# Kernel tuning notes

Hardware: AMD Instinct MI355X
Metric: run time of the kernel (lower is better)

## Reference

```python
import jax, jax.numpy as jnp
import numpy as np

B, N, E = 16, 2048, 1_048_576          # graphs, residues per graph, total edges
IN_C, DIM, OUT_C, ENC_H, N_ATOMS = 256, 128, 6, 100, 20
NT = B * N


def setup_inputs() -> dict:
    key = jax.random.key(0)
    ks = jax.random.split(key, 24)
    s = 0.02
    x_res = jax.random.normal(ks[0], (NT, IN_C), jnp.float32)
    coords = jax.random.normal(ks[1], (NT, 3), jnp.float32)
    batch = jnp.repeat(jnp.arange(B, dtype=jnp.int32), N)
    src = jax.random.randint(ks[2], (E,), 0, NT, dtype=jnp.int32)
    dst = (src // N) * N + jax.random.randint(ks[3], (E,), 0, N, dtype=jnp.int32)
    edge_index = jnp.stack([src, dst])  # intra-graph edges, global node ids
    return {
        'x_res': x_res, 'coords': coords,
        'edge_index': edge_index, 'batch': batch,
        'bn_gamma': jnp.ones((IN_C,), jnp.float32),
        'bn_beta': jnp.zeros((IN_C,), jnp.float32),
        'W1': s * jax.random.normal(ks[4], (IN_C, 2 * DIM), jnp.float32),
        'b1': jnp.zeros((2 * DIM,), jnp.float32),
        'W2': s * jax.random.normal(ks[5], (2 * DIM, DIM), jnp.float32),
        'b2': jnp.zeros((DIM,), jnp.float32),
        'W3': s * jax.random.normal(ks[6], (DIM, N_ATOMS), jnp.float32),
        'b3': jnp.zeros((N_ATOMS,), jnp.float32),
        'embed': s * jax.random.normal(ks[7], (N_ATOMS + 1, DIM), jnp.float32),
        'W_msg': s * jax.random.normal(ks[8], (DIM, DIM), jnp.float32),
        'b_msg': jnp.zeros((DIM,), jnp.float32),
        'w_coor': s * jax.random.normal(ks[9], (DIM, 3), jnp.float32),
        'A1': s * jax.random.normal(ks[10], (DIM, ENC_H), jnp.float32),
        'a1': jnp.zeros((ENC_H,), jnp.float32),
        'A2': s * jax.random.normal(ks[11], (ENC_H, OUT_C), jnp.float32),
        'a2': jnp.zeros((OUT_C,), jnp.float32),
        'dyt_alpha': jnp.float32(0.5),
        'dyt_w': jnp.ones((OUT_C,), jnp.float32),
        'dyt_b': jnp.zeros((OUT_C,), jnp.float32),
    }


def reference(x_res, coords, edge_index, batch,
              bn_gamma, bn_beta, W1, b1, W2, b2, W3, b3,
              embed, W_msg, b_msg, w_coor,
              A1, a1, A2, a2, dyt_alpha, dyt_w, dyt_b):
    gelu = lambda v: jax.nn.gelu(v, approximate=False)
    # BatchNorm1d (train-mode batch stats, biased var, eps=1e-5); dropout is identity in eval
    mu = x_res.mean(0)
    var = x_res.var(0)
    xn = (x_res - mu) / jnp.sqrt(var + 1e-5) * bn_gamma + bn_beta
    # input2atomids MLP -> argmax atom ids
    h1 = gelu(xn @ W1 + b1)
    h2 = gelu(h1 @ W2 + b2)
    logits = h2 @ W3 + b3
    ids = jnp.argmax(logits, axis=-1)          # [NT]
    ids_b = ids.reshape(B, N)                  # equal-sized graphs -> no padding needed
    coords_b = coords.reshape(B, N, 3)
    # vectorized edge-list -> dense per-graph adjacency scatter
    g = batch[edge_index[0]]                   # graph id per edge
    ls = edge_index[0] - g * N                 # local src index
    ld = edge_index[1] - g * N                 # local dst index
    same = batch[edge_index[1]] == g           # keep intra-graph edges only
    adj = jnp.zeros((B, N, N), jnp.bool_).at[g, ls, ld].max(same)
    # GotenNet stand-in: embed atom ids, one adjacency-masked aggregation layer
    emb_ids = jnp.where(ids_b < 0, N_ATOMS, ids_b)   # -1 pad -> pad embedding row
    h = embed[emb_ids]                          # [B,N,DIM]
    adjf = adj.astype(h.dtype)
    deg = jnp.maximum(adjf.sum(-1, keepdims=True), 1.0)
    m = jnp.einsum('bij,bjd->bid', adjf, h) / deg
    hout = gelu((h + m) @ W_msg + b_msg)        # invariant features [B,N,DIM]
    coors_out = coords_b + jnp.tanh(hout @ w_coor)
    # un-pad / flatten back to node list, then out_angles head
    z = hout.reshape(NT, DIM)
    t = gelu(z @ A1 + a1)
    t = gelu(t @ A2 + a2)
    t = jnp.tanh(dyt_alpha * t) * dyt_w + dyt_b  # DynamicTanh (channels_last)
    angles = jnp.tanh(t)                         # [NT, OUT_C]
    return angles, z, coors_out
```

## Files before the change

### kernel.cpp

```cpp
#include <hip/hip_runtime.h>
#include <hip/hip_bf16.h>
#include <math.h>

#define Bg 16
#define Nn 2048
#define Ee (1<<20)
#define NT (Bg*Nn)
#define INC 256
#define DIMd 128
#define OUTC 6
#define ENCH 100
#define NATOMS 20

typedef __attribute__((ext_vector_type(8))) short bf16x8;
typedef __attribute__((ext_vector_type(4))) float f32x4;

__device__ __forceinline__ float gelu_f(float x){
    return 0.5f*x*(1.0f+erff(x*0.70710678118654752440f));
}
__device__ __forceinline__ unsigned short f2b(float f){
    __hip_bfloat16 h = __float2bfloat16(f);
    return *(unsigned short*)&h;
}
__device__ __forceinline__ float b2f(unsigned short u){
    unsigned v = ((unsigned)u)<<16;
    return __uint_as_float(v);
}
__device__ __forceinline__ void splitf(float v, unsigned short& hi, unsigned short& lo){
    unsigned short h = f2b(v);
    hi = h; lo = f2b(v - b2f(h));
}

__global__ __launch_bounds__(256) void prep0_k(const float* __restrict__ x,
    float* __restrict__ stats, const float* __restrict__ W1,
    const float* __restrict__ W2, const float* __restrict__ Wm,
    const float* __restrict__ A1, short* __restrict__ w1th, short* __restrict__ w1tl,
    short* __restrict__ w2th, short* __restrict__ w2tl,
    short* __restrict__ wmth, short* __restrict__ wmtl,
    short* __restrict__ a1th, short* __restrict__ a1tl)
{
    int bx = blockIdx.x, tid = threadIdx.x;
    if(bx < 256){
        int c = tid;
        int r0 = bx * 128;
        const float* p = x + (size_t)r0*INC + c;
        float s = 0.f, s2 = 0.f;
        #pragma unroll 8
        for(int r=0;r<128;r++){ float v = p[(size_t)r*INC]; s += v; s2 += v*v; }
        atomicAdd(&stats[c], s);
        atomicAdd(&stats[INC+c], s2);
    } else {
        int gid = (bx-256)*256 + tid;
        unsigned short hi, lo;
        for(int l=gid;l<65536;l+=16384){ int n=l>>8,k=l&255;
            splitf(W1[(size_t)k*256+n],hi,lo); w1th[l]=(short)hi; w1tl[l]=(short)lo; }
        for(int l=gid;l<32768;l+=16384){ int n=l>>8,k=l&255;
            splitf(W2[(size_t)k*128+n],hi,lo); w2th[l]=(short)hi; w2tl[l]=(short)lo; }
        for(int l=gid;l<16384;l+=16384){ int n=l>>7,k=l&127;
            splitf(Wm[(size_t)k*128+n],hi,lo); wmth[l]=(short)hi; wmtl[l]=(short)lo; }
        for(int l=gid;l<16384;l+=16384){ int n=l>>7,k=l&127;
            float v=(n<ENCH)? A1[(size_t)k*ENCH+n] : 0.f;
            splitf(v,hi,lo); a1th[l]=(short)hi; a1tl[l]=(short)lo; }
    }
}

__global__ __launch_bounds__(256) void gemm1_adj_k(const float* __restrict__ x,
    const float* __restrict__ stats, const float* __restrict__ gamma,
    const float* __restrict__ beta, const short* __restrict__ w1th,
    const short* __restrict__ w1tl, const float* __restrict__ b1,
    unsigned short* __restrict__ h1h, unsigned short* __restrict__ h1l,
    const int* __restrict__ ei, unsigned* __restrict__ mask)
{
    __shared__ float sc[256], sh[256];
    __shared__ short sAh[64*40], sAl[64*40];
    __shared__ short sBh[256*40], sBl[256*40];
    int tid = threadIdx.x;
    {
        float mu  = stats[tid]*(1.0f/NT);
        float var = stats[256+tid]*(1.0f/NT) - mu*mu;
        float s = gamma[tid]/sqrtf(var + 1e-5f);
        sc[tid] = s; sh[tid] = beta[tid] - mu*s;
    }
    int row0 = blockIdx.x*64;
    int lane = tid&63, w = tid>>6;
    int ln = lane&15, quad = lane>>4;
    int m0w = (w&1)*32, n0b = (w>>1)*128;
    f32x4 acc[2][8];
    #pragma unroll
    for(int i=0;i<2;i++)
        #pragma unroll
        for(int j=0;j<8;j++) acc[i][j] = (f32x4){0.f,0.f,0.f,0.f};
    __syncthreads();
    for(int k0=0;k0<256;k0+=32){
        #pragma unroll
        for(int i=0;i<2;i++){
            int id = tid + i*256; int r = id>>3, kq = (id&7)*4;
            float4 vx = *(const float4*)&x[(size_t)(row0+r)*256 + k0+kq];
            int k = k0+kq;
            float v0 = vx.x*sc[k]+sh[k],   v1 = vx.y*sc[k+1]+sh[k+1];
            float v2 = vx.z*sc[k+2]+sh[k+2], v3 = vx.w*sc[k+3]+sh[k+3];
            ushort4 hi, lo;
            splitf(v0,hi.x,lo.x); splitf(v1,hi.y,lo.y);
            splitf(v2,hi.z,lo.z); splitf(v3,hi.w,lo.w);
            *(ushort4*)&sAh[r*40+kq] = hi;
            *(ushort4*)&sAl[r*40+kq] = lo;
        }
        #pragma unroll
        for(int i=0;i<8;i++){
            int id = tid + i*256; int plane = id>>10, cid = id&1023;
            int r = cid>>2, c = cid&3;
            const short* src = (plane? w1tl : w1th) + (size_t)r*256 + k0 + c*8;
            short* dst = (plane? sBl : sBh) + r*40 + c*8;
            *(bf16x8*)dst = *(const bf16x8*)src;
        }
        __syncthreads();
        bf16x8 ah[2], al[2];
        #pragma unroll
        for(int tm=0;tm<2;tm++){
            ah[tm] = *(const bf16x8*)&sAh[(m0w+tm*16+ln)*40 + quad*8];
            al[tm] = *(const bf16x8*)&sAl[(m0w+tm*16+ln)*40 + quad*8];
        }
        #pragma unroll
        for(int tn=0;tn<8;tn++){
            bf16x8 bh = *(const bf16x8*)&sBh[(n0b+tn*16+ln)*40 + quad*8];
            bf16x8 bl = *(const bf16x8*)&sBl[(n0b+tn*16+ln)*40 + quad*8];
            #pragma unroll
            for(int tm=0;tm<2;tm++){
                acc[tm][tn] = __builtin_amdgcn_mfma_f32_16x16x32_bf16(al[tm], bh, acc[tm][tn], 0,0,0);
                acc[tm][tn] = __builtin_amdgcn_mfma_f32_16x16x32_bf16(ah[tm], bl, acc[tm][tn], 0,0,0);
                acc[tm][tn] = __builtin_amdgcn_mfma_f32_16x16x32_bf16(ah[tm], bh, acc[tm][tn], 0,0,0);
            }
        }
        __syncthreads();
    }
    #pragma unroll
    for(int tn=0;tn<8;tn++){
        int col = n0b + tn*16 + ln;
        float bias = b1[col];
        #pragma unroll
        for(int tm=0;tm<2;tm++){
            int rowb = row0 + m0w + tm*16 + quad*4;
            #pragma unroll
            for(int r=0;r<4;r++){
                float hv = gelu_f(acc[tm][tn][r] + bias);
                unsigned short hi, lo;
                splitf(hv, hi, lo);
                h1h[(size_t)(rowb+r)*256 + col] = hi;
                h1l[(size_t)(rowb+r)*256 + col] = lo;
            }
        }
    }
    int ebase = blockIdx.x*2048;
    #pragma unroll
    for(int i=0;i<8;i++){
        int e = ebase + i*256 + tid;
        int s = ei[e], d = ei[Ee+e];
        if((s>>11) == (d>>11)){
            int ld = d & (Nn-1);
            atomicOr(&mask[(size_t)s*64 + (ld>>5)], 1u<<(ld&31));
        }
    }
}

__global__ __launch_bounds__(256) void gemm23_mfma(
    const unsigned short* __restrict__ h1h, const unsigned short* __restrict__ h1l,
    const short* __restrict__ w2th, const short* __restrict__ w2tl,
    const float* __restrict__ b2, const float* __restrict__ W3,
    const float* __restrict__ b3, int* __restrict__ ids)
{
    __shared__ short sAh[64*40], sAl[64*40];
    __shared__ short sBh[128*40], sBl[128*40];
    __shared__ float h2s[64*132];
    __shared__ float lgs[64*20];
    int tid = threadIdx.x;
    int row0 = blockIdx.x*64;
    int lane = tid&63, w = tid>>6;
    int ln = lane&15, quad = lane>>4;
    int m0w = (w&1)*32, n0w = (w>>1)*64;
    f32x4 acc[2][4];
    #pragma unroll
    for(int i=0;i<2;i++)
        #pragma unroll
        for(int j=0;j<4;j++) acc[i][j] = (f32x4){0.f,0.f,0.f,0.f};
    for(int k0=0;k0<256;k0+=32){
        #pragma unroll
        for(int i=0;i<2;i++){
            int id = tid + i*256; int plane = id>>8, cid = id&255;
            int r = cid>>2, c = cid&3;
            const unsigned short* src = (plane? h1l : h1h)
                                        + (size_t)(row0+r)*256 + k0 + c*8;
            short* dst = (plane? sAl : sAh) + r*40 + c*8;
            *(bf16x8*)dst = *(const bf16x8*)src;
        }
        #pragma unroll
        for(int i=0;i<4;i++){
            int id = tid + i*256; int plane = id>>9, cid = id&511;
            int r = cid>>2, c = cid&3;
            const short* src = (plane? w2tl : w2th) + (size_t)r*256 + k0 + c*8;
            short* dst = (plane? sBl : sBh) + r*40 + c*8;
            *(bf16x8*)dst = *(const bf16x8*)src;
        }
        __syncthreads();
        bf16x8 ah[2], al[2];
        #pragma unroll
        for(int tm=0;tm<2;tm++){
            ah[tm] = *(const bf16x8*)&sAh[(m0w+tm*16+ln)*40 + quad*8];
            al[tm] = *(const bf16x8*)&sAl[(m0w+tm*16+ln)*40 + quad*8];
        }
        #pragma unroll
        for(int tn=0;tn<4;tn++){
            bf16x8 bh = *(const bf16x8*)&sBh[(n0w+tn*16+ln)*40 + quad*8];
            bf16x8 bl = *(const bf16x8*)&sBl[(n0w+tn*16+ln)*40 + quad*8];
            #pragma unroll
            for(int tm=0;tm<2;tm++){
                acc[tm][tn] = __builtin_amdgcn_mfma_f32_16x16x32_bf16(al[tm], bh, acc[tm][tn], 0,0,0);
                acc[tm][tn] = __builtin_amdgcn_mfma_f32_16x16x32_bf16(ah[tm], bl, acc[tm][tn], 0,0,0);
                acc[tm][tn] = __builtin_amdgcn_mfma_f32_16x16x32_bf16(ah[tm], bh, acc[tm][tn], 0,0,0);
            }
        }
        __syncthreads();
    }
    #pragma unroll
    for(int tn=0;tn<4;tn++){
        int col = n0w + tn*16 + ln;
        float bias = b2[col];
        #pragma unroll
        for(int tm=0;tm<2;tm++){
            int rb = m0w + tm*16 + quad*4;
            #pragma unroll
            for(int r=0;r<4;r++)
                h2s[(rb+r)*132 + col] = gelu_f(acc[tm][tn][r] + bias);
        }
    }
    float* w3s = (float*)sBh;
    for(int l=tid;l<2560;l+=256) w3s[l] = W3[l];
    __syncthreads();
    int n = tid>>2, q = tid&3;
    float lg[5] = {};
    #pragma unroll 4
    for(int k=0;k<128;k++){
        float h = h2s[n*132+k];
        #pragma unroll
        for(int a=0;a<5;a++) lg[a] += h*w3s[k*20 + q*5 + a];
    }
    #pragma unroll
    for(int a=0;a<5;a++) lgs[n*20 + q*5 + a] = lg[a] + b3[q*5+a];
    __syncthreads();
    if(tid<64){
        float best = lgs[tid*20]; int bi = 0;
        #pragma unroll
        for(int a=1;a<20;a++){ float v2 = lgs[tid*20+a]; if(v2>best){best=v2;bi=a;} }
        ids[row0+tid] = bi;
    }
}

__global__ __launch_bounds__(256) void msg3_k(
    const int* __restrict__ ids, const unsigned* __restrict__ mask,
    const float* __restrict__ embed,
    const short* __restrict__ wmth, const short* __restrict__ wmtl,
    const float* __restrict__ b_msg, const float* __restrict__ w_coor,
    const short* __restrict__ a1th, const short* __restrict__ a1tl,
    const float* __restrict__ a1v, const float* __restrict__ A2,
    const float* __restrict__ a2v, const float* __restrict__ dalpha,
    const float* __restrict__ dw, const float* __restrict__ db,
    const float* __restrict__ coords, float* __restrict__ out_ang,
    float* __restrict__ out_z, float* __restrict__ out_co)
{
    __shared__ unsigned short v_bf[64*136];
    __shared__ unsigned short houts[64*136];
    __shared__ __align__(16) unsigned char arena[20480];
    __shared__ float s_bm[128], s_wc[384], s_A2[624], s_a1[104];
    __shared__ float s_dyt[16], s_a2[8];

    unsigned*       ind = (unsigned*)arena;
    unsigned char*  sid = arena + 5120;
    float*          emb = (float*)(arena + 7168);
    short*          sBh = (short*)arena;
    short*          sBl = (short*)(arena + 10240);

    int tid = threadIdx.x;
    int row0 = blockIdx.x*64;
    int g = blockIdx.x>>5, tile = blockIdx.x&31;
    int lane = tid&63, w = tid>>6;
    int ln = lane&15, quad = lane>>4;
    int m0w = (w&1)*32, n0w = (w>>1)*64;

    for(int l=tid;l<NATOMS*128;l+=256) emb[l] = embed[l];
    #pragma unroll
    for(int i=0;i<8;i++){ int j = tid + i*256; sid[j] = (unsigned char)ids[g*Nn + j]; }
    if(tid<128) s_bm[tid] = b_msg[tid];
    if(tid<104) s_a1[tid] = (tid<ENCH) ? a1v[tid] : 0.f;
    for(int l=tid;l<384;l+=256) s_wc[l] = w_coor[l];
    for(int l=tid;l<624;l+=256) s_A2[l] = (l<600) ? A2[l] : 0.f;
    if(tid==0)  s_dyt[0] = dalpha[0];
    if(tid<6){ s_dyt[1+tid] = dw[tid]; s_dyt[8+tid] = db[tid]; }
    if(tid<8)  s_a2[tid] = (tid<6) ? a2v[tid] : 0.f;

    int node = tid>>2, p = tid&3;
    const unsigned* mrow = &mask[((size_t)(row0 + node))*64 + p*16];
    uint4 mm0 = *(const uint4*)&mrow[0];
    uint4 mm1 = *(const uint4*)&mrow[4];
    uint4 mm2 = *(const uint4*)&mrow[8];
    uint4 mm3 = *(const uint4*)&mrow[12];
    __syncthreads();

    for(int wp=w; wp<32; wp+=4){
        int a = sid[wp*64 + lane];
        #pragma unroll
        for(int atom=0; atom<NATOMS; atom++){
            unsigned long long bm = __ballot(a==atom);
            if(lane<2) ind[atom*64 + wp*2 + lane] = (unsigned)(bm >> (32*lane));
        }
    }
    __syncthreads();

    unsigned mw[16];
    *(uint4*)&mw[0]=mm0; *(uint4*)&mw[4]=mm1; *(uint4*)&mw[8]=mm2; *(uint4*)&mw[12]=mm3;
    int degi = 0;
    #pragma unroll
    for(int w2=0;w2<16;w2++) degi += __popc(mw[w2]);
    float cnt[NATOMS];
    #pragma unroll
    for(int a=0;a<NATOMS;a++){
        int c = 0;
        const unsigned* ia = &ind[a*64 + p*16];
        #pragma unroll
        for(int w2=0;w2<16;w2++) c += __popc(mw[w2] & ia[w2]);
        cnt[a] = (float)c;
    }
    #pragma unroll
    for(int a=0;a<NATOMS;a++){
        cnt[a] += __shfl_xor(cnt[a],1,64);
        cnt[a] += __shfl_xor(cnt[a],2,64);
    }
    float deg = (float)degi;
    deg += __shfl_xor(deg,1,64);
    deg += __shfl_xor(deg,2,64);

    {
        float inv = 1.0f / fmaxf(deg, 1.0f);
        int oid = sid[tile*64 + node];
        int d0 = p*32;
        float vv[32];
        #pragma unroll
        for(int d=0;d<32;d++) vv[d]=0.f;
        #pragma unroll
        for(int a=0;a<NATOMS;a++){
            float ca = cnt[a];
            const float* ea = &emb[a*128 + d0];
            #pragma unroll
            for(int d=0;d<32;d+=4){
                float4 e = *(const float4*)&ea[d];
                vv[d]+=ca*e.x; vv[d+1]+=ca*e.y; vv[d+2]+=ca*e.z; vv[d+3]+=ca*e.w;
            }
        }
        const float* eo = &emb[oid*128 + d0];
        unsigned short* dst = &v_bf[node*136 + d0];
        #pragma unroll
        for(int d=0;d<32;d+=4){
            float4 e = *(const float4*)&eo[d];
            ushort4 o;
            o.x = f2b(e.x + vv[d]*inv);
            o.y = f2b(e.y + vv[d+1]*inv);
            o.z = f2b(e.z + vv[d+2]*inv);
            o.w = f2b(e.w + vv[d+3]*inv);
            *(ushort4*)&dst[d] = o;
        }
    }
    __syncthreads();

    f32x4 acc[2][4];
    #pragma unroll
    for(int i=0;i<2;i++)
        #pragma unroll
        for(int j=0;j<4;j++) acc[i][j] = (f32x4){0.f,0.f,0.f,0.f};
    for(int k0=0;k0<128;k0+=32){
        #pragma unroll
        for(int i=0;i<4;i++){
            int id = tid + i*256; int plane = id>>9, cid = id&511;
            int r = cid>>2, c = cid&3;
            const short* src = (plane? wmtl : wmth) + (size_t)r*128 + k0 + c*8;
            short* dst = (plane? sBl : sBh) + r*40 + c*8;
            *(bf16x8*)dst = *(const bf16x8*)src;
        }
        __syncthreads();
        bf16x8 av[2];
        #pragma unroll
        for(int tm=0;tm<2;tm++)
            av[tm] = *(const bf16x8*)&v_bf[(m0w+tm*16+ln)*136 + k0 + quad*8];
        #pragma unroll
        for(int tn=0;tn<4;tn++){
            bf16x8 bh = *(const bf16x8*)&sBh[(n0w+tn*16+ln)*40 + quad*8];
            bf16x8 bl = *(const bf16x8*)&sBl[(n0w+tn*16+ln)*40 + quad*8];
            #pragma unroll
            for(int tm=0;tm<2;tm++){
                acc[tm][tn] = __builtin_amdgcn_mfma_f32_16x16x32_bf16(av[tm], bl, acc[tm][tn], 0,0,0);
                acc[tm][tn] = __builtin_amdgcn_mfma_f32_16x16x32_bf16(av[tm], bh, acc[tm][tn], 0,0,0);
            }
        }
        __syncthreads();
    }
    #pragma unroll
    for(int tn=0;tn<4;tn++){
        int col = n0w + tn*16 + ln;
        float bias = s_bm[col];
        #pragma unroll
        for(int tm=0;tm<2;tm++){
            int mb2 = m0w + tm*16 + quad*4;
            #pragma unroll
            for(int r=0;r<4;r++){
                float hv = gelu_f(acc[tm][tn][r] + bias);
                out_z[(size_t)(row0+mb2+r)*128 + col] = hv;
                houts[(mb2+r)*136 + col] = f2b(hv);
            }
        }
    }
    __syncthreads();

    {
        float d0=0.f, d1=0.f, d2=0.f;
        int kb = p*32;
        #pragma unroll
        for(int k=0;k<32;k+=4){
            ushort4 hv = *(const ushort4*)&houts[node*136 + kb + k];
            float h0=b2f(hv.x),h1=b2f(hv.y),h2=b2f(hv.z),h3=b2f(hv.w);
            const float* wc = &s_wc[(kb+k)*3];
            d0 += h0*wc[0]+h1*wc[3]+h2*wc[6]+h3*wc[9];
            d1 += h0*wc[1]+h1*wc[4]+h2*wc[7]+h3*wc[10];
            d2 += h0*wc[2]+h1*wc[5]+h2*wc[8]+h3*wc[11];
        }
        d0 += __shfl_xor(d0,1,64); d0 += __shfl_xor(d0,2,64);
        d1 += __shfl_xor(d1,1,64); d1 += __shfl_xor(d1,2,64);
        d2 += __shfl_xor(d2,1,64); d2 += __shfl_xor(d2,2,64);
        if(p==0){
            size_t o = (size_t)(row0+node)*3;
            out_co[o+0] = coords[o+0] + tanhf(d0);
            out_co[o+1] = coords[o+1] + tanhf(d1);
            out_co[o+2] = coords[o+2] + tanhf(d2);
        }
    }

    f32x4 acc2[2][4];
    #pragma unroll
    for(int i=0;i<2;i++)
        #pragma unroll
        for(int j=0;j<4;j++) acc2[i][j] = (f32x4){0.f,0.f,0.f,0.f};
    for(int k0=0;k0<128;k0+=32){
        __syncthreads();
        #pragma unroll
        for(int i=0;i<4;i++){
            int id = tid + i*256; int plane = id>>9, cid = id&511;
            int r = cid>>2, c = cid&3;
            const short* src = (plane? a1tl : a1th) + (size_t)r*128 + k0 + c*8;
            short* dst = (plane? sBl : sBh) + r*40 + c*8;
            *(bf16x8*)dst = *(const bf16x8*)src;
        }
        __syncthreads();
        bf16x8 ah[2];
        #pragma unroll
        for(int tm=0;tm<2;tm++)
            ah[tm] = *(const bf16x8*)&houts[(m0w+tm*16+ln)*136 + k0 + quad*8];
        #pragma unroll
        for(int tn=0;tn<4;tn++){
            bf16x8 bh = *(const bf16x8*)&sBh[(n0w+tn*16+ln)*40 + quad*8];
            bf16x8 bl = *(const bf16x8*)&sBl[(n0w+tn*16+ln)*40 + quad*8];
            #pragma unroll
            for(int tm=0;tm<2;tm++){
                acc2[tm][tn] = __builtin_amdgcn_mfma_f32_16x16x32_bf16(ah[tm], bl, acc2[tm][tn], 0,0,0);
                acc2[tm][tn] = __builtin_amdgcn_mfma_f32_16x16x32_bf16(ah[tm], bh, acc2[tm][tn], 0,0,0);
            }
        }
    }
    __syncthreads();
    unsigned short* t1s = houts;
    #pragma unroll
    for(int tn=0;tn<4;tn++){
        int col = n0w + tn*16 + ln;
        if(col < 104){
            float bias = s_a1[col];
            #pragma unroll
            for(int tm=0;tm<2;tm++){
                int mb2 = m0w + tm*16 + quad*4;
                #pragma unroll
                for(int r=0;r<4;r++)
                    t1s[(mb2+r)*104 + col] = f2b(gelu_f(acc2[tm][tn][r] + bias));
            }
        }
    }
    __syncthreads();

    {
        int g0 = (p<2) ? p*7 : 14+(p-2)*6;
        int gcount = (p<2) ? 7 : 6;
        float s[6] = {0.f,0.f,0.f,0.f,0.f,0.f};
        for(int gg=0; gg<gcount; gg++){
            int kb = (g0+gg)*4;
            ushort4 tv = *(const ushort4*)&t1s[node*104 + kb];
            float u0=b2f(tv.x), u1=b2f(tv.y), u2=b2f(tv.z), u3=b2f(tv.w);
            #pragma unroll
            for(int j=0;j<6;j++)
                s[j] += u0*s_A2[kb*6+j] + u1*s_A2[(kb+1)*6+j]
                      + u2*s_A2[(kb+2)*6+j] + u3*s_A2[(kb+3)*6+j];
        }
        #pragma unroll
        for(int j=0;j<6;j++){ s[j]+=__shfl_xor(s[j],1,64); s[j]+=__shfl_xor(s[j],2,64); }
        if(p<2){
            size_t o = (size_t)(row0+node)*6 + p*3;
            #pragma unroll
            for(int jj=0;jj<3;jj++){
                int j = p*3+jj;
                float t2v = gelu_f(s[j] + s_a2[j]);
                float uu = tanhf(s_dyt[0]*t2v)*s_dyt[1+j] + s_dyt[8+j];
                out_ang[o+jj] = tanhf(uu);
            }
        }
    }
}

extern "C" void kernel_launch(void* const* d_in, const int* in_sizes, int n_in,
                              void* d_out, int out_size, void* d_ws, size_t ws_size,
                              hipStream_t stream) {
    const float* x      = (const float*)d_in[0];
    const float* coords = (const float*)d_in[1];
    const int*   ei     = (const int*)d_in[2];
    const float* gamma  = (const float*)d_in[4];
    const float* beta   = (const float*)d_in[5];
    const float* W1     = (const float*)d_in[6];
    const float* b1     = (const float*)d_in[7];
    const float* W2     = (const float*)d_in[8];
    const float* b2     = (const float*)d_in[9];
    const float* W3     = (const float*)d_in[10];
    const float* b3     = (const float*)d_in[11];
    const float* embed  = (const float*)d_in[12];
    const float* W_msg  = (const float*)d_in[13];
    const float* b_msg  = (const float*)d_in[14];
    const float* w_coor = (const float*)d_in[15];
    const float* A1     = (const float*)d_in[16];
    const float* a1v    = (const float*)d_in[17];
    const float* A2     = (const float*)d_in[18];
    const float* a2v    = (const float*)d_in[19];
    const float* dalpha = (const float*)d_in[20];
    const float* dw     = (const float*)d_in[21];
    const float* db     = (const float*)d_in[22];

    char* ws = (char*)d_ws;
    int*      ids   = (int*)ws;
    float*    stats = (float*)(ws + 131072);
    short*    w1th  = (short*)(ws + 262144);
    short*    w1tl  = w1th + 65536;
    short*    w2th  = w1tl + 65536;
    short*    w2tl  = w2th + 32768;
    short*    wmth  = w2tl + 32768;
    short*    wmtl  = wmth + 16384;
    short*    a1th  = wmtl + 16384;
    short*    a1tl  = a1th + 16384;
    unsigned* mask  = (unsigned*)(ws + (1<<20));
    unsigned short* h1h = (unsigned short*)(ws + (size_t)10*1048576);
    unsigned short* h1l = (unsigned short*)(ws + (size_t)27*1048576);

    float* out_ang = (float*)d_out;
    float* out_z   = out_ang + (size_t)NT*OUTC;
    float* out_co  = out_z   + (size_t)NT*DIMd;

    hipMemsetAsync(stats, 0, 2*INC*sizeof(float), stream);
    hipMemsetAsync(mask, 0, (size_t)NT*64*sizeof(unsigned), stream);
    prep0_k<<<320, 256, 0, stream>>>(x, stats, W1, W2, W_msg, A1,
        w1th, w1tl, w2th, w2tl, wmth, wmtl, a1th, a1tl);
    gemm1_adj_k<<<512, 256, 0, stream>>>(x, stats, gamma, beta, w1th, w1tl, b1,
        h1h, h1l, ei, mask);
    gemm23_mfma<<<512, 256, 0, stream>>>(h1h, h1l, w2th, w2tl, b2, W3, b3, ids);
    msg3_k<<<512, 256, 0, stream>>>(ids, mask, embed, wmth, wmtl, b_msg, w_coor,
        a1th, a1tl, a1v, A2, a2v, dalpha, dw, db, coords, out_ang, out_z, out_co);
}
```

Before: 271.9 us.

## Bin edges per 64-node tile and build adjacency masks in LDS; register-prefetch GEMM tiles

Measured after the change: 253.9 us. -6.6%, faster.

```diff
diff --git a/kernel.cpp b/kernel.cpp
--- a/kernel.cpp
+++ b/kernel.cpp
@@ -11,6 +11,7 @@
 #define OUTC 6
 #define ENCH 100
 #define NATOMS 20
+#define BINCAP 3072
 
 typedef __attribute__((ext_vector_type(8))) short bf16x8;
 typedef __attribute__((ext_vector_type(4))) float f32x4;
@@ -64,12 +65,13 @@
     }
 }
 
-__global__ __launch_bounds__(256) void gemm1_adj_k(const float* __restrict__ x,
+__global__ __launch_bounds__(256) void gemm1_scat_k(const float* __restrict__ x,
     const float* __restrict__ stats, const float* __restrict__ gamma,
     const float* __restrict__ beta, const short* __restrict__ w1th,
     const short* __restrict__ w1tl, const float* __restrict__ b1,
     unsigned short* __restrict__ h1h, unsigned short* __restrict__ h1l,
-    const int* __restrict__ ei, unsigned* __restrict__ mask)
+    const int* __restrict__ ei, unsigned* __restrict__ ecnt,
+    unsigned* __restrict__ earena)
 {
     __shared__ float sc[256], sh[256];
     __shared__ short sAh[64*40], sAl[64*40];
@@ -90,15 +92,23 @@
     for(int i=0;i<2;i++)
         #pragma unroll
         for(int j=0;j<8;j++) acc[i][j] = (f32x4){0.f,0.f,0.f,0.f};
+
+    float4 xa[2]; bf16x8 wb[8];
+    #pragma unroll
+    for(int i=0;i<2;i++){ int id=tid+i*256; int r=id>>3,kq=(id&7)*4;
+        xa[i] = *(const float4*)&x[(size_t)(row0+r)*256 + kq]; }
+    #pragma unroll
+    for(int i=0;i<8;i++){ int id=tid+i*256; int plane=id>>10,cid=id&1023;
+        int r=cid>>2,c=cid&3;
+        wb[i] = *(const bf16x8*)((plane? w1tl:w1th) + (size_t)r*256 + c*8); }
     __syncthreads();
     for(int k0=0;k0<256;k0+=32){
         #pragma unroll
         for(int i=0;i<2;i++){
             int id = tid + i*256; int r = id>>3, kq = (id&7)*4;
-            float4 vx = *(const float4*)&x[(size_t)(row0+r)*256 + k0+kq];
             int k = k0+kq;
-            float v0 = vx.x*sc[k]+sh[k],   v1 = vx.y*sc[k+1]+sh[k+1];
-            float v2 = vx.z*sc[k+2]+sh[k+2], v3 = vx.w*sc[k+3]+sh[k+3];
+            float v0 = xa[i].x*sc[k]+sh[k],   v1 = xa[i].y*sc[k+1]+sh[k+1];
+            float v2 = xa[i].z*sc[k+2]+sh[k+2], v3 = xa[i].w*sc[k+3]+sh[k+3];
             ushort4 hi, lo;
             splitf(v0,hi.x,lo.x); splitf(v1,hi.y,lo.y);
             splitf(v2,hi.z,lo.z); splitf(v3,hi.w,lo.w);
@@ -109,11 +119,18 @@
         for(int i=0;i<8;i++){
             int id = tid + i*256; int plane = id>>10, cid = id&1023;
             int r = cid>>2, c = cid&3;
-            const short* src = (plane? w1tl : w1th) + (size_t)r*256 + k0 + c*8;
-            short* dst = (plane? sBl : sBh) + r*40 + c*8;
-            *(bf16x8*)dst = *(const bf16x8*)src;
-        }
-        __syncthreads();
+            *(bf16x8*)((plane? sBl : sBh) + r*40 + c*8) = wb[i];
+        }
+        __syncthreads();
+        if(k0 < 224){
+            #pragma unroll
+            for(int i=0;i<2;i++){ int id=tid+i*256; int r=id>>3,kq=(id&7)*4;
+                xa[i] = *(const float4*)&x[(size_t)(row0+r)*256 + k0+32+kq]; }
+            #pragma unroll
+            for(int i=0;i<8;i++){ int id=tid+i*256; int plane=id>>10,cid=id&1023;
+                int r=cid>>2,c=cid&3;
+                wb[i] = *(const bf16x8*)((plane? w1tl:w1th) + (size_t)r*256 + k0+32 + c*8); }
+        }
         bf16x8 ah[2], al[2];
         #pragma unroll
         for(int tm=0;tm<2;tm++){
@@ -150,14 +167,38 @@
             }
         }
     }
-    int ebase = blockIdx.x*2048;
-    #pragma unroll
-    for(int i=0;i<8;i++){
-        int e = ebase + i*256 + tid;
-        int s = ei[e], d = ei[Ee+e];
-        if((s>>11) == (d>>11)){
-            int ld = d & (Nn-1);
-            atomicOr(&mask[(size_t)s*64 + (ld>>5)], 1u<<(ld&31));
+    if(blockIdx.x < 128){
+        __syncthreads();
+        unsigned* lcnt  = (unsigned*)sAh;
+        unsigned* gbase = ((unsigned*)sAh) + 512;
+        for(int l=tid; l<512; l+=256) lcnt[l] = 0;
+        __syncthreads();
+        int ebase = blockIdx.x * 8192;
+        #pragma unroll 8
+        for(int i=0;i<32;i++){
+            int e = ebase + i*256 + tid;
+            int s = ei[e], d = ei[Ee+e];
+            if((s>>11)==(d>>11)) atomicAdd(&lcnt[s>>6], 1u);
+        }
+        __syncthreads();
+        for(int l=tid; l<512; l+=256){
+            unsigned c = lcnt[l];
+            gbase[l] = c ? atomicAdd(&ecnt[l], c) : 0u;
+            lcnt[l] = 0;
+        }
+        __syncthreads();
+        #pragma unroll 8
+        for(int i=0;i<32;i++){
+            int e = ebase + i*256 + tid;
+            int s = ei[e], d = ei[Ee+e];
+            if((s>>11)==(d>>11)){
+                int bin = s>>6;
+                unsigned r = atomicAdd(&lcnt[bin], 1u);
+                unsigned pos = gbase[bin] + r;
+                if(pos < BINCAP)
+                    earena[(size_t)bin*BINCAP + pos] =
+                        ((unsigned)(s&63)<<11) | (unsigned)(d&2047);
+            }
         }
     }
 }
@@ -182,25 +223,42 @@
     for(int i=0;i<2;i++)
         #pragma unroll
         for(int j=0;j<4;j++) acc[i][j] = (f32x4){0.f,0.f,0.f,0.f};
+
+    bf16x8 ha[2], wb[4];
+    #pragma unroll
+    for(int i=0;i<2;i++){ int id=tid+i*256; int plane=id>>8,cid=id&255;
+        int r=cid>>2,c=cid&3;
+        ha[i] = *(const bf16x8*)((const short*)(plane? h1l : h1h)
+                                 + (size_t)(row0+r)*256 + c*8); }
+    #pragma unroll
+    for(int i=0;i<4;i++){ int id=tid+i*256; int plane=id>>9,cid=id&511;
+        int r=cid>>2,c=cid&3;
+        wb[i] = *(const bf16x8*)((plane? w2tl:w2th) + (size_t)r*256 + c*8); }
     for(int k0=0;k0<256;k0+=32){
         #pragma unroll
         for(int i=0;i<2;i++){
             int id = tid + i*256; int plane = id>>8, cid = id&255;
             int r = cid>>2, c = cid&3;
-            const unsigned short* src = (plane? h1l : h1h)
-                                        + (size_t)(row0+r)*256 + k0 + c*8;
-            short* dst = (plane? sAl : sAh) + r*40 + c*8;
-            *(bf16x8*)dst = *(const bf16x8*)src;
+            *(bf16x8*)((plane? sAl : sAh) + r*40 + c*8) = ha[i];
         }
         #pragma unroll
         for(int i=0;i<4;i++){
             int id = tid + i*256; int plane = id>>9, cid = id&511;
             int r = cid>>2, c = cid&3;
-            const short* src = (plane? w2tl : w2th) + (size_t)r*256 + k0 + c*8;
-            short* dst = (plane? sBl : sBh) + r*40 + c*8;
-            *(bf16x8*)dst = *(const bf16x8*)src;
-        }
-        __syncthreads();
+            *(bf16x8*)((plane? sBl : sBh) + r*40 + c*8) = wb[i];
+        }
+        __syncthreads();
+        if(k0 < 224){
+            #pragma unroll
+            for(int i=0;i<2;i++){ int id=tid+i*256; int plane=id>>8,cid=id&255;
+                int r=cid>>2,c=cid&3;
+                ha[i] = *(const bf16x8*)((const short*)(plane? h1l : h1h)
+                                         + (size_t)(row0+r)*256 + k0+32 + c*8); }
+            #pragma unroll
+            for(int i=0;i<4;i++){ int id=tid+i*256; int plane=id>>9,cid=id&511;
+                int r=cid>>2,c=cid&3;
+                wb[i] = *(const bf16x8*)((plane? w2tl:w2th) + (size_t)r*256 + k0+32 + c*8); }
+        }
         bf16x8 ah[2], al[2];
         #pragma unroll
         for(int tm=0;tm<2;tm++){
@@ -255,8 +313,8 @@
 }
 
 __global__ __launch_bounds__(256) void msg3_k(
-    const int* __restrict__ ids, const unsigned* __restrict__ mask,
-    const float* __restrict__ embed,
+    const int* __restrict__ ids, const unsigned* __restrict__ ecnt,
+    const unsigned* __restrict__ earena, const float* __restrict__ embed,
     const short* __restrict__ wmth, const short* __restrict__ wmtl,
     const float* __restrict__ b_msg, const float* __restrict__ w_coor,
     const short* __restrict__ a1th, const short* __restrict__ a1tl,
@@ -268,18 +326,20 @@
 {
     __shared__ unsigned short v_bf[64*136];
     __shared__ unsigned short houts[64*136];
-    __shared__ __align__(16) unsigned char arena[20480];
+    __shared__ __align__(16) unsigned char arena[33792];
     __shared__ float s_bm[128], s_wc[384], s_A2[624], s_a1[104];
     __shared__ float s_dyt[16], s_a2[8];
 
-    unsigned*       ind = (unsigned*)arena;
-    unsigned char*  sid = arena + 5120;
-    float*          emb = (float*)(arena + 7168);
-    short*          sBh = (short*)arena;
-    short*          sBl = (short*)(arena + 10240);
+    unsigned*       lmask = (unsigned*)arena;
+    unsigned*       ind   = (unsigned*)(arena + 16384);
+    unsigned char*  sid   = arena + 21504;
+    float*          emb   = (float*)(arena + 23552);
+    short*          sBh   = (short*)arena;
+    short*          sBl   = (short*)(arena + 10240);
 
     int tid = threadIdx.x;
-    int row0 = blockIdx.x*64;
+    int bin = blockIdx.x;
+    int row0 = bin*64;
     int g = blockIdx.x>>5, tile = blockIdx.x&31;
     int lane = tid&63, w = tid>>6;
     int ln = lane&15, quad = lane>>4;
@@ -288,6 +348,8 @@
     for(int l=tid;l<NATOMS*128;l+=256) emb[l] = embed[l];
     #pragma unroll
     for(int i=0;i<8;i++){ int j = tid + i*256; sid[j] = (unsigned char)ids[g*Nn + j]; }
+    #pragma unroll
+    for(int i=0;i<16;i++) lmask[tid + i*256] = 0;
     if(tid<128) s_bm[tid] = b_msg[tid];
     if(tid<104) s_a1[tid] = (tid<ENCH) ? a1v[tid] : 0.f;
     for(int l=tid;l<384;l+=256) s_wc[l] = w_coor[l];
@@ -295,13 +357,7 @@
     if(tid==0)  s_dyt[0] = dalpha[0];
     if(tid<6){ s_dyt[1+tid] = dw[tid]; s_dyt[8+tid] = db[tid]; }
     if(tid<8)  s_a2[tid] = (tid<6) ? a2v[tid] : 0.f;
-
-    int node = tid>>2, p = tid&3;
-    const unsigned* mrow = &mask[((size_t)(row0 + node))*64 + p*16];
-    uint4 mm0 = *(const uint4*)&mrow[0];
-    uint4 mm1 = *(const uint4*)&mrow[4];
-    uint4 mm2 = *(const uint4*)&mrow[8];
-    uint4 mm3 = *(const uint4*)&mrow[12];
+    int nb = min((int)ecnt[bin], BINCAP);
     __syncthreads();
 
     for(int wp=w; wp<32; wp+=4){
@@ -312,10 +368,22 @@
             if(lane<2) ind[atom*64 + wp*2 + lane] = (unsigned)(bm >> (32*lane));
         }
     }
-    __syncthreads();
-
+    for(int i=tid; i<nb; i+=256){
+        unsigned wv = earena[(size_t)bin*BINCAP + i];
+        int sl = wv>>11, dl = wv & 2047;
+        atomicOr(&lmask[sl*64 + (dl>>5)], 1u<<(dl&31));
+    }
+    __syncthreads();
+
+    int node = tid>>2, p = tid&3;
     unsigned mw[16];
-    *(uint4*)&mw[0]=mm0; *(uint4*)&mw[4]=mm1; *(uint4*)&mw[8]=mm2; *(uint4*)&mw[12]=mm3;
+    {
+        const unsigned* mrow = &lmask[node*64 + p*16];
+        *(uint4*)&mw[0]  = *(const uint4*)&mrow[0];
+        *(uint4*)&mw[4]  = *(const uint4*)&mrow[4];
+        *(uint4*)&mw[8]  = *(const uint4*)&mrow[8];
+        *(uint4*)&mw[12] = *(const uint4*)&mrow[12];
+    }
     int degi = 0;
     #pragma unroll
     for(int w2=0;w2<16;w2++) degi += __popc(mw[w2]);
@@ -546,6 +614,7 @@
     char* ws = (char*)d_ws;
     int*      ids   = (int*)ws;
     float*    stats = (float*)(ws + 131072);
+    unsigned* ecnt  = (unsigned*)(ws + 131072 + 2048);
     short*    w1th  = (short*)(ws + 262144);
     short*    w1tl  = w1th + 65536;
     short*    w2th  = w1tl + 65536;
@@ -554,7 +623,7 @@
     short*    wmtl  = wmth + 16384;
     short*    a1th  = wmtl + 16384;
     short*    a1tl  = a1th + 16384;
-    unsigned* mask  = (unsigned*)(ws + (1<<20));
+    unsigned* earena = (unsigned*)(ws + (1<<20));
     unsigned short* h1h = (unsigned short*)(ws + (size_t)10*1048576);
     unsigned short* h1l = (unsigned short*)(ws + (size_t)27*1048576);
 
@@ -562,13 +631,13 @@
     float* out_z   = out_ang + (size_t)NT*OUTC;
     float* out_co  = out_z   + (size_t)NT*DIMd;
 
-    hipMemsetAsync(stats, 0, 2*INC*sizeof(float), stream);
-    hipMemsetAsync(mask, 0, (size_t)NT*64*sizeof(unsigned), stream);
+    hipMemsetAsync(stats, 0, 4096, stream);
     prep0_k<<<320, 256, 0, stream>>>(x, stats, W1, W2, W_msg, A1,
         w1th, w1tl, w2th, w2tl, wmth, wmtl, a1th, a1tl);
-    gemm1_adj_k<<<512, 256, 0, stream>>>(x, stats, gamma, beta, w1th, w1tl, b1,
-        h1h, h1l, ei, mask);
+    gemm1_scat_k<<<512, 256, 0, stream>>>(x, stats, gamma, beta, w1th, w1tl, b1,
+        h1h, h1l, ei, ecnt, earena);
     gemm23_mfma<<<512, 256, 0, stream>>>(h1h, h1l, w2th, w2tl, b2, W3, b3, ids);
-    msg3_k<<<512, 256, 0, stream>>>(ids, mask, embed, wmth, wmtl, b_msg, w_coor,
-        a1th, a1tl, a1v, A2, a2v, dalpha, dw, db, coords, out_ang, out_z, out_co);
-}
+    msg3_k<<<512, 256, 0, stream>>>(ids, ecnt, earena, embed, wmth, wmtl, b_msg,
+        w_coor, a1th, a1tl, a1v, A2, a2v, dalpha, dw, db, coords,
+        out_ang, out_z, out_co);
+}
```
